# Kernel optimization log

Hardware: AMD Instinct MI355X
Metric: run time of the kernel (lower is better)

## Reference

```python
import jax, jax.numpy as jnp
import numpy as np

B, N, C_IN = 4, 4096, 64
DIM = 64
NKP = 15
K = 32               # neighbor_limits
CONV_RADIUS = 0.1 * 2.0   # conv_radius * rigid_scale (is_deform=False)
KERNEL_RADIUS = 0.12
RECEP = 1.2          # kernel_point_receptive_radius
TRANS_DIM = 128
INF = 1000000.0


def _square_distance(src, dst):
    # src [B,N,3], dst [B,M,3] -> [B,N,M]
    d = -2.0 * jnp.einsum('bnc,bmc->bnm', src, dst)
    d = d + jnp.sum(src * src, -1)[:, :, None]
    d = d + jnp.sum(dst * dst, -1)[:, None, :]
    return d


def _query_ball(xyz, radius):
    # xyz [B,N,3] -> neighbor idx [B,N,K]; out-of-radius mapped to N (shadow)
    n = xyz.shape[1]
    sq = _square_distance(xyz, xyz)
    idx = jnp.broadcast_to(jnp.arange(n, dtype=jnp.int32), sq.shape)
    idx = jnp.where(sq > radius * radius, n, idx)
    idx = jnp.sort(idx, axis=-1)[:, :, :K]
    return idx


def _index_points(points_bcn, idx, pad_val):
    # points [B,C,N], idx [B,N,K] -> [B,N,K,C]; index N hits shadow row = pad_val
    p = jnp.transpose(points_bcn, (0, 2, 1))          # [B,N,C]
    shadow = jnp.full((p.shape[0], 1, p.shape[2]), pad_val, p.dtype)
    p = jnp.concatenate([p, shadow], axis=1)          # [B,N+1,C]
    b_idx = jnp.arange(p.shape[0])[:, None, None]
    return p[b_idx, idx]                              # [B,N,K,C]


def setup_inputs() -> dict:
    key = jax.random.key(0)
    ks = jax.random.split(key, 12)
    pos = jax.random.uniform(ks[0], (B, 3, N), dtype=jnp.float32)
    feat = jax.random.normal(ks[1], (B, C_IN, N), dtype=jnp.float32)
    # kernel points: center point at origin, rest inside kernel_radius ball ('center' mode)
    kp_rest = jax.random.uniform(ks[2], (3, NKP - 1), minval=-KERNEL_RADIUS,
                                 maxval=KERNEL_RADIUS, dtype=jnp.float32)
    kp_pos = jnp.concatenate([jnp.zeros((3, 1), jnp.float32), kp_rest], axis=1)  # [3,NKP]
    s = 0.05
    cb_w = jax.random.normal(ks[3], (DIM, C_IN), jnp.float32) * s
    cb_b = jax.random.normal(ks[4], (DIM,), jnp.float32) * s
    kp_weight = jax.random.normal(ks[5], (NKP, DIM, DIM), jnp.float32) * s
    kp_bias = jax.random.normal(ks[6], (DIM,), jnp.float32) * s
    ce_w = jax.random.normal(ks[7], (C_IN, DIM), jnp.float32) * s
    ce_b = jax.random.normal(ks[8], (C_IN,), jnp.float32) * s
    f1_w = jax.random.normal(ks[9], (2 * DIM, 2 * DIM), jnp.float32) * s
    f1_b = jnp.zeros((2 * DIM,), jnp.float32)
    f2_w = jax.random.normal(ks[10], (TRANS_DIM, 2 * DIM), jnp.float32) * s
    f2_b = jnp.zeros((TRANS_DIM,), jnp.float32)
    return dict(pos=pos, feat=feat, kp_pos=kp_pos, cb_w=cb_w, cb_b=cb_b,
                kp_weight=kp_weight, kp_bias=kp_bias, ce_w=ce_w, ce_b=ce_b,
                f1_w=f1_w, f1_b=f1_b, f2_w=f2_w, f2_b=f2_b)


def reference(pos, feat, kp_pos, cb_w, cb_b, kp_weight, kp_bias, ce_w, ce_b,
              f1_w, f1_b, f2_w, f2_b):
    xyz = jnp.transpose(jax.lax.stop_gradient(pos), (0, 2, 1))       # [B,N,3]
    neighbor_idx = _query_ball(xyz, CONV_RADIUS)                     # [B,N,K]
    # NOTE: with is_deform=False the original code does NOT subtract the center
    # position; rel_neighbor_pos is the absolute gathered positions.
    neighbor_pos = jnp.transpose(_index_points(pos, neighbor_idx, INF),
                                 (0, 3, 1, 2))                        # [B,3,N,K]
    feat0 = jnp.einsum('oc,bcn->bon', cb_w, feat) + cb_b[None, :, None]
    neighbor_feat = _index_points(feat0, neighbor_idx, 0.0)           # [B,N,K,DIM]

    kp_pos_deform = kp_pos.reshape(1, 3, 1, NKP) + 0.0                # offset = 0
    diff = neighbor_pos[..., None] - kp_pos_deform[:, :, :, None, :]  # [B,3,N,K,NKP]
    sq_d = jnp.sum(diff * diff, axis=1)                               # [B,N,K,NKP]
    w = jnp.clip(1.0 - jnp.sqrt(sq_d) / RECEP, 0.0)                   # [B,N,K,NKP]
    w = jnp.transpose(w, (0, 1, 3, 2))                                # [B,N,NKP,K]
    weighted = jnp.einsum('bnpk,bnkc->bnpc', w, neighbor_feat)        # [B,N,NKP,DIM]
    out = jnp.einsum('bnpc,pcd->bnd', weighted, kp_weight) + kp_bias  # [B,N,DIM]
    out = jax.nn.relu(jnp.transpose(out, (0, 2, 1)))                  # [B,DIM,N]
    out = jax.nn.relu(jnp.einsum('oc,bcn->bon', ce_w, out)
                      + ce_b[None, :, None] + feat)                   # [B,C_IN,N]

    fuse_in = jnp.concatenate(
        [jnp.transpose(weighted, (0, 3, 1, 2)),                       # [B,DIM,N,NKP]
         jnp.broadcast_to(out[..., None], (B, DIM, N, NKP))], axis=1) # [B,2DIM,N,NKP]
    h = jax.nn.relu(jnp.einsum('oc,bcnk->bonk', f1_w, fuse_in)
                    + f1_b[None, :, None, None])
    fuse = jax.nn.relu(jnp.einsum('oc,bcnk->bonk', f2_w, h)
                       + f2_b[None, :, None, None])                   # [B,TRANS_DIM,N,NKP]
    return out, kp_pos_deform, fuse
```

## Files before the change

kernel.cpp:

```cpp
#include <hip/hip_runtime.h>
#include <hip/hip_bf16.h>
#include <stdint.h>

#define NPTS 4096
#define NB   4
#define KNN  32
#define NKPT 15

#define OFF_IDX      0ULL
#define OFF_FEAT0    2097152ULL
#define OFF_WEIGHTED 6292480ULL
#define OFF_HO       37749760ULL
#define OFF_W1P      41944064ULL
#define OFF_W2P      41976832ULL
#define OFF_KPWP     42009600ULL

#define OUT_OFF_OUT  0
#define OUT_OFF_KP   1048576
#define OUT_OFF_FUSE 1048621

#define SBU(u) ((u) ^ (((u) >> 3) & 7))

typedef __attribute__((ext_vector_type(8))) short short8v;
typedef __attribute__((ext_vector_type(4))) float f32x4;

__device__ __forceinline__ unsigned short bf16b(float f) {
  __hip_bfloat16 h = __float2bfloat16(f);
  return *(unsigned short*)&h;
}
__device__ __forceinline__ unsigned pkbf(float lo, float hi) {
  return (unsigned)bf16b(lo) | ((unsigned)bf16b(hi) << 16);
}
__device__ __forceinline__ float bflo(unsigned u) { return __uint_as_float(u << 16); }
__device__ __forceinline__ float bfhi(unsigned u) { return __uint_as_float(u & 0xffff0000u); }

__global__ __launch_bounds__(256) void k012(const float* __restrict__ pos,
                                            const float* __restrict__ feat,
                                            const float* __restrict__ cb_w,
                                            const float* __restrict__ cb_b,
                                            const float* __restrict__ f1_w,
                                            const float* __restrict__ f2_w,
                                            const float* __restrict__ kpw,
                                            const float* __restrict__ kp_pos,
                                            int* __restrict__ idx_ws,
                                            float* __restrict__ feat0,
                                            unsigned short* __restrict__ w1p,
                                            unsigned short* __restrict__ w2p,
                                            unsigned short* __restrict__ kpwp,
                                            float* __restrict__ out_kp) {
  __shared__ float cbt[64 * 65];
  const int blk = blockIdx.x;
  if (blk < 4096) {
    const int w = threadIdx.x >> 6, lane = threadIdx.x & 63;
    const int pt = blk * 4 + w;
    const int b = pt >> 12, n = pt & 4095;
    const float* px = pos + (size_t)b * 3 * NPTS;
    const float x0 = px[n], y0 = px[NPTS + n], z0 = px[2 * NPTS + n];
    const float ssrcf = x0 * x0 + y0 * y0 + z0 * z0;
    const double x0d = (double)x0, y0d = (double)y0, z0d = (double)z0;
    const double ssrcd = x0d * x0d + y0d * y0d + z0d * z0d;
    const double RAD = 0.1 * 2.0;
    const double R2 = RAD * RAD;
    const float R2f = (float)R2;
    int cnt = 0;
    int* op = idx_ws + (size_t)pt * KNN;
    for (int ch = 0; ch < 64; ++ch) {
      const int j = ch * 64 + lane;
      const float xj = px[j], yj = px[NPTS + j], zj = px[2 * NPTS + j];
      const float dotf = x0 * xj + y0 * yj + z0 * zj;
      const float sdf  = xj * xj + yj * yj + zj * zj;
      const float sqf  = -2.0f * dotf + ssrcf + sdf;
      const float diff = sqf - R2f;
      bool keep;
      if (__builtin_expect(fabsf(diff) <= 1e-4f, 0)) {
        const double xd = (double)xj, yd = (double)yj, zd = (double)zj;
        const double dd = -2.0 * (x0d * xd + y0d * yd + z0d * zd) + ssrcd
                          + (xd * xd + yd * yd + zd * zd);
        keep = !(dd > R2);
      } else {
        keep = (diff <= 0.0f);
      }
      const unsigned long long m = __ballot(keep);
      if (keep) {
        const int p = cnt + (int)__popcll(m & ((1ULL << lane) - 1ULL));
        if (p < KNN) op[p] = j;
      }
      cnt += (int)__popcll(m);
      if (cnt >= KNN) break;
    }
    const int s = cnt + lane;
    if (s < KNN) op[s] = NPTS;
    return;
  }
  if (blk < 8192) {
    const int t = threadIdx.x;
    #pragma unroll
    for (int q = 0; q < 16; ++q) {
      const int idx = q * 256 + t;
      const int d = idx >> 6, c = idx & 63;
      cbt[c * 65 + d] = cb_w[idx];
    }
    __syncthreads();
    const int ptl = t >> 6, d = t & 63;
    const int pt = (blk - 4096) * 4 + ptl;
    const int b = pt >> 12, n = pt & 4095;
    const float* fp = feat + (size_t)b * 64 * NPTS + n;
    float acc = 0.f;
    #pragma unroll
    for (int c = 0; c < 64; ++c) acc = fmaf(cbt[c * 65 + d], fp[(size_t)c * NPTS], acc);
    acc += cb_b[d];
    feat0[((size_t)b * (NPTS + 1) + n) * 64 + d] = acc;
    return;
  }
  int t = (blk - 8192) * 256 + threadIdx.x;
  if (t < 32768) {
    const int w = t >> 14;
    const int i = t & 16383;
    const int j = i & 7, l = (i >> 3) & 63, kc = (i >> 9) & 3, ot = i >> 11;
    const int o = ot * 16 + (l & 15);
    const int k = kc * 32 + (l >> 4) * 8 + j;
    const float* src = w ? f2_w : f1_w;
    unsigned short* dst = w ? w2p : w1p;
    dst[i] = bf16b(src[o * 128 + k]);
    return;
  }
  t -= 32768;
  if (t < 61440) {
    const int j = t & 7, l = (t >> 3) & 63, nt = (t >> 9) & 3, kc = t >> 11;
    const int k = kc * 32 + (l >> 4) * 8 + j;
    const int d = nt * 16 + (l & 15);
    kpwp[t] = bf16b(kpw[(size_t)k * 64 + d]);
    return;
  }
  t -= 61440;
  if (t < NB * 64) { int b = t >> 6, d = t & 63; feat0[((size_t)b * (NPTS + 1) + NPTS) * 64 + d] = 0.f; return; }
  t -= NB * 64;
  if (t < 45) out_kp[t] = kp_pos[t];
}

__global__ __launch_bounds__(64) void k3_weighted(const float* __restrict__ pos,
                                                  const int* __restrict__ idx_ws,
                                                  const float* __restrict__ feat0,
                                                  const float* __restrict__ kp_pos,
                                                  unsigned short* __restrict__ wbf) {
  __shared__ int   nidx[KNN];
  __shared__ float npx[KNN], npy[KNN], npz[KNN];
  __shared__ float kp[48];
  __shared__ float wl[KNN * 16];
  const int lane = threadIdx.x;
  const int pt = blockIdx.x;
  const int b = pt >> 12;
  if (lane < 45) kp[lane] = kp_pos[lane];
  if (lane < KNN) {
    const int ki = idx_ws[(size_t)pt * KNN + lane];
    nidx[lane] = ki;
    const bool v = ki < NPTS;
    const float* px = pos + (size_t)b * 3 * NPTS;
    npx[lane] = v ? px[ki] : 1000000.0f;
    npy[lane] = v ? px[NPTS + ki] : 1000000.0f;
    npz[lane] = v ? px[2 * NPTS + ki] : 1000000.0f;
  }
  __syncthreads();
  #pragma unroll
  for (int r = 0; r < 8; ++r) {
    const int i = r * 64 + lane;
    const int k = i >> 4, p = i & 15;
    float wv = 0.f;
    if (p < 15) {
      const float dx = npx[k] - kp[p];
      const float dy = npy[k] - kp[15 + p];
      const float dz = npz[k] - kp[30 + p];
      const float d2 = dx * dx + dy * dy + dz * dz;
      wv = fmaxf(1.0f - sqrtf(d2) / 1.2f, 0.f);
    }
    wl[i] = wv;
  }
  __syncthreads();
  float acc[16];
  #pragma unroll
  for (int p = 0; p < 16; ++p) acc[p] = 0.f;
  const float* f0 = feat0 + (size_t)b * (NPTS + 1) * 64 + lane;
  for (int k = 0; k < KNN; ++k) {
    const float f = f0[(size_t)nidx[k] * 64];
    #pragma unroll
    for (int q = 0; q < 4; ++q) {
      const float4 w4 = *(const float4*)&wl[k * 16 + q * 4];
      acc[q * 4 + 0] = fmaf(w4.x, f, acc[q * 4 + 0]);
      acc[q * 4 + 1] = fmaf(w4.y, f, acc[q * 4 + 1]);
      acc[q * 4 + 2] = fmaf(w4.z, f, acc[q * 4 + 2]);
      acc[q * 4 + 3] = fmaf(w4.w, f, acc[q * 4 + 3]);
    }
  }
  unsigned short* wp = wbf + (size_t)pt * NKPT * 64 + lane;
  #pragma unroll
  for (int p = 0; p < 15; ++p) wp[(size_t)p * 64] = bf16b(acc[p]);
}

__global__ __launch_bounds__(256) void k45(const unsigned short* __restrict__ wbf,
                                           const unsigned short* __restrict__ kpwp,
                                           const float* __restrict__ kp_bias,
                                           const float* __restrict__ ce_w,
                                           const float* __restrict__ ce_b,
                                           const float* __restrict__ feat,
                                           const unsigned short* __restrict__ w1p,
                                           const float* __restrict__ f1_b,
                                           float* __restrict__ out,
                                           unsigned short* __restrict__ hOb) {
  __shared__ float r0[64 * 65];
  __shared__ float cwt[64 * 64];
  __shared__ unsigned short outT[64 * 74];
  const int t = threadIdx.x;
  const int b = blockIdx.x >> 6;
  const int n0 = (blockIdx.x & 63) * 64;
  const int wv = t >> 6, lane = t & 63;
  #pragma unroll
  for (int q = 0; q < 16; ++q) {
    const int idx = q * 256 + t;
    cwt[idx] = ce_w[(idx & 63) * 64 + (idx >> 6)];
  }
  const short8v* kf = (const short8v*)kpwp;
  f32x4 acc[4];
  #pragma unroll
  for (int nt = 0; nt < 4; ++nt) acc[nt] = (f32x4){0.f, 0.f, 0.f, 0.f};
  const int m0 = b * 4096 + n0 + wv * 16;
  const unsigned short* ap = wbf + (size_t)(m0 + (lane & 15)) * 960 + (lane >> 4) * 8;
  #pragma unroll 6
  for (int kc = 0; kc < 30; ++kc) {
    const short8v a = *(const short8v*)&ap[kc * 32];
    #pragma unroll
    for (int nt = 0; nt < 4; ++nt)
      acc[nt] = __builtin_amdgcn_mfma_f32_16x16x32_bf16(a, kf[(kc * 4 + nt) * 64 + lane], acc[nt], 0, 0, 0);
  }
  const int rl = wv * 16 + (lane >> 4) * 4;
  #pragma unroll
  for (int nt = 0; nt < 4; ++nt) {
    const int d = nt * 16 + (lane & 15);
    const float bv = kp_bias[d];
    #pragma unroll
    for (int r = 0; r < 4; ++r)
      r0[(rl + r) * 65 + d] = fmaxf(acc[nt][r] + bv, 0.f);
  }
  __syncthreads();
  const int nl = t & 63, og = t >> 6;
  float facc[16];
  #pragma unroll
  for (int j = 0; j < 16; ++j) facc[j] = 0.f;
  for (int c = 0; c < 64; ++c) {
    const float x = r0[nl * 65 + c];
    #pragma unroll
    for (int q = 0; q < 4; ++q) {
      const float4 w4 = *(const float4*)&cwt[c * 64 + og * 16 + q * 4];
      facc[q * 4 + 0] = fmaf(w4.x, x, facc[q * 4 + 0]);
      facc[q * 4 + 1] = fmaf(w4.y, x, facc[q * 4 + 1]);
      facc[q * 4 + 2] = fmaf(w4.z, x, facc[q * 4 + 2]);
      facc[q * 4 + 3] = fmaf(w4.w, x, facc[q * 4 + 3]);
    }
  }
  #pragma unroll
  for (int q = 0; q < 4; ++q) {
    const float4 cb4 = *(const float4*)&ce_b[og * 16 + q * 4];
    const float cbv[4] = {cb4.x, cb4.y, cb4.z, cb4.w};
    #pragma unroll
    for (int j = 0; j < 4; ++j) {
      const int o = og * 16 + q * 4 + j;
      const float fv = feat[((size_t)b * 64 + o) * 4096 + n0 + nl];
      const float v = fmaxf((facc[q * 4 + j] + cbv[j]) + fv, 0.f);
      out[((size_t)b * 64 + o) * 4096 + n0 + nl] = v;
      outT[o * 74 + nl] = bf16b(v);
    }
  }
  __syncthreads();
  const short8v* w1f = (const short8v*)w1p;
  f32x4 hacc[8];
  #pragma unroll
  for (int ot = 0; ot < 8; ++ot) hacc[ot] = (f32x4){0.f, 0.f, 0.f, 0.f};
  const int nw = lane & 15;
  #pragma unroll
  for (int kc2 = 0; kc2 < 2; ++kc2) {
    short8v bfr;
    #pragma unroll
    for (int j = 0; j < 8; ++j)
      bfr[j] = (short)outT[(kc2 * 32 + (lane >> 4) * 8 + j) * 74 + wv * 16 + nw];
    #pragma unroll
    for (int ot = 0; ot < 8; ++ot)
      hacc[ot] = __builtin_amdgcn_mfma_f32_16x16x32_bf16(w1f[(ot * 4 + 2 + kc2) * 64 + lane], bfr, hacc[ot], 0, 0, 0);
  }
  const int rb = (lane >> 4) * 4;
  unsigned short* hp = hOb + ((size_t)b * 4096 + n0 + wv * 16 + nw) * 128;
  #pragma unroll
  for (int ot = 0; ot < 8; ++ot) {
    const int o0 = ot * 16 + rb;
    const float4 b1 = *(const float4*)&f1_b[o0];
    uint2 pk;
    pk.x = pkbf(hacc[ot][0] + b1.x, hacc[ot][1] + b1.y);
    pk.y = pkbf(hacc[ot][2] + b1.z, hacc[ot][3] + b1.w);
    *(uint2*)&hp[o0] = pk;
  }
}

__global__ __launch_bounds__(256, 2) void k6_fuse(const unsigned short* __restrict__ wbf,
                                                  const unsigned short* __restrict__ hOb,
                                                  const unsigned short* __restrict__ w1p,
                                                  const unsigned short* __restrict__ w2p,
                                                  const float* __restrict__ f2_b,
                                                  float* __restrict__ fuse) {
  __shared__ __attribute__((aligned(16))) unsigned short SB[16384];
  __shared__ __attribute__((aligned(8))) unsigned short hOS[12 * 128];
  const int t = threadIdx.x;
  const int blk = blockIdx.x;
  const int b = blk / 480;
  const int ml0 = (blk - b * 480) * 128;
  const size_t M0 = (size_t)blk * 128;
  const int wv = t >> 6, lane = t & 63;
  const short8v* w1f = (const short8v*)w1p;
  const short8v* w2f = (const short8v*)w2p;

  short8v w1r[16];
  #pragma unroll
  for (int ot = 0; ot < 8; ++ot)
    #pragma unroll
    for (int kc = 0; kc < 2; ++kc)
      w1r[ot * 2 + kc] = w1f[(ot * 4 + kc) * 64 + lane];

  #pragma unroll
  for (int q = 0; q < 4; ++q) {
    const int chunk = q * 256 + t;
    const int m = chunk >> 3, a = chunk & 7;
    const uint4 pk = *(const uint4*)&wbf[(M0 + m) * 64 + a * 8];
    const int kc = a >> 2, hi = a & 3;
    const int u = ((m >> 4) * 4 + kc) * 64 + hi * 16 + (m & 15);
    *(uint4*)&SB[SBU(u) * 8] = pk;
  }
  const int nmin = ml0 / 15;
  #pragma unroll
  for (int q = 0; q < 3; ++q) {
    const int idx = q * 256 + t;
    const int row = idx >> 6, pr = idx & 63;
    int n = nmin + row;
    if (n > 4095) n = 4095;
    ((unsigned*)hOS)[idx] = ((const unsigned*)(hOb + ((size_t)b * 4096 + n) * 128))[pr];
  }
  __syncthreads();

  short8v xf[4];
  #pragma unroll
  for (int mt = 0; mt < 2; ++mt)
    #pragma unroll
    for (int kc = 0; kc < 2; ++kc) {
      const int u = ((wv * 2 + mt) * 4 + kc) * 64 + lane;
      xf[mt * 2 + kc] = *(const short8v*)&SB[SBU(u) * 8];
    }

  const int rb = (lane >> 4) * 4;
  const int dnA = (ml0 + wv * 32 + (lane & 15)) / 15 - nmin;
  const int dnB = (ml0 + wv * 32 + 16 + (lane & 15)) / 15 - nmin;
  f32x4 acc[8][2];
  #pragma unroll
  for (int ot = 0; ot < 8; ++ot) {
    const uint2 pa = *(const uint2*)&hOS[dnA * 128 + ot * 16 + rb];
    const uint2 pb = *(const uint2*)&hOS[dnB * 128 + ot * 16 + rb];
    acc[ot][0] = (f32x4){bflo(pa.x), bfhi(pa.x), bflo(pa.y), bfhi(pa.y)};
    acc[ot][1] = (f32x4){bflo(pb.x), bfhi(pb.x), bflo(pb.y), bfhi(pb.y)};
  }
  short8v w2a[16];
  #pragma unroll
  for (int i = 0; i < 16; ++i) w2a[i] = w2f[i * 64 + lane];

  #pragma unroll
  for (int kc = 0; kc < 2; ++kc) {
    #pragma unroll
    for (int ot = 0; ot < 8; ++ot) {
      acc[ot][0] = __builtin_amdgcn_mfma_f32_16x16x32_bf16(w1r[ot * 2 + kc], xf[kc],     acc[ot][0], 0, 0, 0);
      acc[ot][1] = __builtin_amdgcn_mfma_f32_16x16x32_bf16(w1r[ot * 2 + kc], xf[2 + kc], acc[ot][1], 0, 0, 0);
    }
  }
  #pragma unroll
  for (int ot = 0; ot < 8; ++ot) {
    const int o0 = ot * 16 + rb;
    const int kc = o0 >> 5, hi = (o0 >> 3) & 3, j0 = o0 & 7;
    #pragma unroll
    for (int mt = 0; mt < 2; ++mt) {
      const f32x4 h = acc[ot][mt];
      const float h0 = fmaxf(h[0], 0.f);
      const float h1 = fmaxf(h[1], 0.f);
      const float h2 = fmaxf(h[2], 0.f);
      const float h3 = fmaxf(h[3], 0.f);
      const int u = ((wv * 2 + mt) * 4 + kc) * 64 + hi * 16 + (lane & 15);
      uint2 pk;
      pk.x = pkbf(h0, h1);
      pk.y = pkbf(h2, h3);
      *(uint2*)&SB[SBU(u) * 8 + j0] = pk;
    }
  }
  short8v w2b[16];
  #pragma unroll
  for (int i = 0; i < 16; ++i) w2b[i] = w2f[(16 + i) * 64 + lane];

  short8v hf[8];
  #pragma unroll
  for (int mt = 0; mt < 2; ++mt)
    #pragma unroll
    for (int kc = 0; kc < 4; ++kc) {
      const int u = ((wv * 2 + mt) * 4 + kc) * 64 + lane;
      hf[mt * 4 + kc] = *(const short8v*)&SB[SBU(u) * 8];
    }
  #pragma unroll
  for (int ot = 0; ot < 8; ++ot) {
    acc[ot][0] = (f32x4){0.f, 0.f, 0.f, 0.f};
    acc[ot][1] = (f32x4){0.f, 0.f, 0.f, 0.f};
  }
  #pragma unroll
  for (int kc = 0; kc < 4; ++kc) {
    #pragma unroll
    for (int ot = 0; ot < 4; ++ot) {
      acc[ot][0] = __builtin_amdgcn_mfma_f32_16x16x32_bf16(w2a[ot * 4 + kc], hf[kc],     acc[ot][0], 0, 0, 0);
      acc[ot][1] = __builtin_amdgcn_mfma_f32_16x16x32_bf16(w2a[ot * 4 + kc], hf[4 + kc], acc[ot][1], 0, 0, 0);
    }
  }
  #pragma unroll
  for (int kc = 0; kc < 4; ++kc) {
    #pragma unroll
    for (int ot = 4; ot < 8; ++ot) {
      acc[ot][0] = __builtin_amdgcn_mfma_f32_16x16x32_bf16(w2b[(ot - 4) * 4 + kc], hf[kc],     acc[ot][0], 0, 0, 0);
      acc[ot][1] = __builtin_amdgcn_mfma_f32_16x16x32_bf16(w2b[(ot - 4) * 4 + kc], hf[4 + kc], acc[ot][1], 0, 0, 0);
    }
  }
  float* fp0 = fuse + (size_t)b * 128 * 61440 + ml0 + wv * 32 + (lane & 15);
  #pragma unroll
  for (int ot = 0; ot < 8; ++ot) {
    const int o0 = ot * 16 + rb;
    const float4 b2 = *(const float4*)&f2_b[o0];
    const float bv[4] = {b2.x, b2.y, b2.z, b2.w};
    #pragma unroll
    for (int mt = 0; mt < 2; ++mt) {
      const f32x4 vacc = acc[ot][mt];
      #pragma unroll
      for (int r = 0; r < 4; ++r)
        fp0[(size_t)(o0 + r) * 61440 + mt * 16] = fmaxf(vacc[r] + bv[r], 0.f);
    }
  }
}

extern "C" void kernel_launch(void* const* d_in, const int* in_sizes, int n_in,
                              void* d_out, int out_size, void* d_ws, size_t ws_size,
                              hipStream_t stream) {
  const float* pos     = (const float*)d_in[0];
  const float* feat    = (const float*)d_in[1];
  const float* kp_pos  = (const float*)d_in[2];
  const float* cb_w    = (const float*)d_in[3];
  const float* cb_b    = (const float*)d_in[4];
  const float* kpw     = (const float*)d_in[5];
  const float* kp_bias = (const float*)d_in[6];
  const float* ce_w    = (const float*)d_in[7];
  const float* ce_b    = (const float*)d_in[8];
  const float* f1_w    = (const float*)d_in[9];
  const float* f1_b    = (const float*)d_in[10];
  const float* f2_w    = (const float*)d_in[11];
  const float* f2_b    = (const float*)d_in[12];
  float* out = (float*)d_out;
  char* ws = (char*)d_ws;
  int*   idx_ws   = (int*)(ws + OFF_IDX);
  float* feat0    = (float*)(ws + OFF_FEAT0);
  unsigned short* wbf  = (unsigned short*)(ws + OFF_WEIGHTED);
  unsigned short* hOb  = (unsigned short*)(ws + OFF_HO);
  unsigned short* w1p  = (unsigned short*)(ws + OFF_W1P);
  unsigned short* w2p  = (unsigned short*)(ws + OFF_W2P);
  unsigned short* kpwp = (unsigned short*)(ws + OFF_KPWP);

  k012<<<8562, 256, 0, stream>>>(pos, feat, cb_w, cb_b, f1_w, f2_w, kpw, kp_pos,
                                 idx_ws, feat0, w1p, w2p, kpwp, out + OUT_OFF_KP);
  k3_weighted<<<16384, 64, 0, stream>>>(pos, idx_ws, feat0, kp_pos, wbf);
  k45<<<256, 256, 0, stream>>>(wbf, kpwp, kp_bias, ce_w, ce_b, feat, w1p, f1_b,
                               out + OUT_OFF_OUT, hOb);
  k6_fuse<<<1920, 256, 0, stream>>>(wbf, hOb, w1p, w2p, f2_b, out + OUT_OFF_FUSE);
}
```

Measured before the change: 140.1 us.

## Split fuse MLP work across waves by output channels instead of point columns

Each wave in k6_fuse now owns a 32-channel slice of the outputs and loops over all 128 point columns of the block, where before it owned 32 columns and all 128 channels. Each wave therefore holds only its slice of the W1 and W2 weight fragments in registers, which lowers register pressure. The hidden activations are written to a separate shared buffer, and a block-wide barrier now sits between the two layers. Output stores also change shape: each lane now writes 16-column row segments across its channel slice.

```diff
diff --git a/kernel.cpp b/kernel.cpp
--- a/kernel.cpp
+++ b/kernel.cpp
@@ -305,6 +305,7 @@
                                                   const float* __restrict__ f2_b,
                                                   float* __restrict__ fuse) {
   __shared__ __attribute__((aligned(16))) unsigned short SB[16384];
+  __shared__ __attribute__((aligned(16))) unsigned short HB[16384];
   __shared__ __attribute__((aligned(8))) unsigned short hOS[12 * 128];
   const int t = threadIdx.x;
   const int blk = blockIdx.x;
@@ -312,15 +313,22 @@
   const int ml0 = (blk - b * 480) * 128;
   const size_t M0 = (size_t)blk * 128;
   const int wv = t >> 6, lane = t & 63;
+  const int cl = lane & 15, rb = (lane >> 4) * 4;
   const short8v* w1f = (const short8v*)w1p;
   const short8v* w2f = (const short8v*)w2p;
 
-  short8v w1r[16];
-  #pragma unroll
-  for (int ot = 0; ot < 8; ++ot)
+  short8v w1a[4];
+  #pragma unroll
+  for (int oi = 0; oi < 2; ++oi)
     #pragma unroll
     for (int kc = 0; kc < 2; ++kc)
-      w1r[ot * 2 + kc] = w1f[(ot * 4 + kc) * 64 + lane];
+      w1a[oi * 2 + kc] = w1f[((wv * 2 + oi) * 4 + kc) * 64 + lane];
+  short8v w2r[8];
+  #pragma unroll
+  for (int oi = 0; oi < 2; ++oi)
+    #pragma unroll
+    for (int kc = 0; kc < 4; ++kc)
+      w2r[oi * 4 + kc] = w2f[((wv * 2 + oi) * 4 + kc) * 64 + lane];
 
   #pragma unroll
   for (int q = 0; q < 4; ++q) {
@@ -342,101 +350,57 @@
   }
   __syncthreads();
 
-  short8v xf[4];
-  #pragma unroll
-  for (int mt = 0; mt < 2; ++mt)
-    #pragma unroll
-    for (int kc = 0; kc < 2; ++kc) {
-      const int u = ((wv * 2 + mt) * 4 + kc) * 64 + lane;
-      xf[mt * 2 + kc] = *(const short8v*)&SB[SBU(u) * 8];
-    }
-
-  const int rb = (lane >> 4) * 4;
-  const int dnA = (ml0 + wv * 32 + (lane & 15)) / 15 - nmin;
-  const int dnB = (ml0 + wv * 32 + 16 + (lane & 15)) / 15 - nmin;
-  f32x4 acc[8][2];
-  #pragma unroll
-  for (int ot = 0; ot < 8; ++ot) {
-    const uint2 pa = *(const uint2*)&hOS[dnA * 128 + ot * 16 + rb];
-    const uint2 pb = *(const uint2*)&hOS[dnB * 128 + ot * 16 + rb];
-    acc[ot][0] = (f32x4){bflo(pa.x), bfhi(pa.x), bflo(pa.y), bfhi(pa.y)};
-    acc[ot][1] = (f32x4){bflo(pb.x), bfhi(pb.x), bflo(pb.y), bfhi(pb.y)};
-  }
-  short8v w2a[16];
-  #pragma unroll
-  for (int i = 0; i < 16; ++i) w2a[i] = w2f[i * 64 + lane];
-
-  #pragma unroll
-  for (int kc = 0; kc < 2; ++kc) {
-    #pragma unroll
-    for (int ot = 0; ot < 8; ++ot) {
-      acc[ot][0] = __builtin_amdgcn_mfma_f32_16x16x32_bf16(w1r[ot * 2 + kc], xf[kc],     acc[ot][0], 0, 0, 0);
-      acc[ot][1] = __builtin_amdgcn_mfma_f32_16x16x32_bf16(w1r[ot * 2 + kc], xf[2 + kc], acc[ot][1], 0, 0, 0);
-    }
-  }
-  #pragma unroll
-  for (int ot = 0; ot < 8; ++ot) {
-    const int o0 = ot * 16 + rb;
-    const int kc = o0 >> 5, hi = (o0 >> 3) & 3, j0 = o0 & 7;
-    #pragma unroll
-    for (int mt = 0; mt < 2; ++mt) {
-      const f32x4 h = acc[ot][mt];
-      const float h0 = fmaxf(h[0], 0.f);
-      const float h1 = fmaxf(h[1], 0.f);
-      const float h2 = fmaxf(h[2], 0.f);
-      const float h3 = fmaxf(h[3], 0.f);
-      const int u = ((wv * 2 + mt) * 4 + kc) * 64 + hi * 16 + (lane & 15);
+  #pragma unroll
+  for (int mt = 0; mt < 8; ++mt) {
+    const int dn = (ml0 + mt * 16 + cl) / 15 - nmin;
+    const uint2 p0 = *(const uint2*)&hOS[dn * 128 + wv * 32 + rb];
+    const uint2 p1 = *(const uint2*)&hOS[dn * 128 + wv * 32 + 16 + rb];
+    f32x4 a0 = (f32x4){bflo(p0.x), bfhi(p0.x), bflo(p0.y), bfhi(p0.y)};
+    f32x4 a1 = (f32x4){bflo(p1.x), bfhi(p1.x), bflo(p1.y), bfhi(p1.y)};
+    const short8v x0 = *(const short8v*)&SB[SBU((mt * 4 + 0) * 64 + lane) * 8];
+    const short8v x1 = *(const short8v*)&SB[SBU((mt * 4 + 1) * 64 + lane) * 8];
+    a0 = __builtin_amdgcn_mfma_f32_16x16x32_bf16(w1a[0], x0, a0, 0, 0, 0);
+    a0 = __builtin_amdgcn_mfma_f32_16x16x32_bf16(w1a[1], x1, a0, 0, 0, 0);
+    a1 = __builtin_amdgcn_mfma_f32_16x16x32_bf16(w1a[2], x0, a1, 0, 0, 0);
+    a1 = __builtin_amdgcn_mfma_f32_16x16x32_bf16(w1a[3], x1, a1, 0, 0, 0);
+    #pragma unroll
+    for (int oi = 0; oi < 2; ++oi) {
+      const f32x4 h = oi ? a1 : a0;
+      const int c0 = wv * 32 + oi * 16 + rb;
+      const int kc = c0 >> 5, hi = (c0 >> 3) & 3, j0 = c0 & 7;
       uint2 pk;
-      pk.x = pkbf(h0, h1);
-      pk.y = pkbf(h2, h3);
-      *(uint2*)&SB[SBU(u) * 8 + j0] = pk;
-    }
-  }
-  short8v w2b[16];
-  #pragma unroll
-  for (int i = 0; i < 16; ++i) w2b[i] = w2f[(16 + i) * 64 + lane];
-
-  short8v hf[8];
-  #pragma unroll
-  for (int mt = 0; mt < 2; ++mt)
-    #pragma unroll
-    for (int kc = 0; kc < 4; ++kc) {
-      const int u = ((wv * 2 + mt) * 4 + kc) * 64 + lane;
-      hf[mt * 4 + kc] = *(const short8v*)&SB[SBU(u) * 8];
-    }
-  #pragma unroll
-  for (int ot = 0; ot < 8; ++ot) {
-    acc[ot][0] = (f32x4){0.f, 0.f, 0.f, 0.f};
-    acc[ot][1] = (f32x4){0.f, 0.f, 0.f, 0.f};
-  }
-  #pragma unroll
-  for (int kc = 0; kc < 4; ++kc) {
-    #pragma unroll
-    for (int ot = 0; ot < 4; ++ot) {
-      acc[ot][0] = __builtin_amdgcn_mfma_f32_16x16x32_bf16(w2a[ot * 4 + kc], hf[kc],     acc[ot][0], 0, 0, 0);
-      acc[ot][1] = __builtin_amdgcn_mfma_f32_16x16x32_bf16(w2a[ot * 4 + kc], hf[4 + kc], acc[ot][1], 0, 0, 0);
-    }
-  }
-  #pragma unroll
-  for (int kc = 0; kc < 4; ++kc) {
-    #pragma unroll
-    for (int ot = 4; ot < 8; ++ot) {
-      acc[ot][0] = __builtin_amdgcn_mfma_f32_16x16x32_bf16(w2b[(ot - 4) * 4 + kc], hf[kc],     acc[ot][0], 0, 0, 0);
-      acc[ot][1] = __builtin_amdgcn_mfma_f32_16x16x32_bf16(w2b[(ot - 4) * 4 + kc], hf[4 + kc], acc[ot][1], 0, 0, 0);
-    }
-  }
-  float* fp0 = fuse + (size_t)b * 128 * 61440 + ml0 + wv * 32 + (lane & 15);
-  #pragma unroll
-  for (int ot = 0; ot < 8; ++ot) {
-    const int o0 = ot * 16 + rb;
-    const float4 b2 = *(const float4*)&f2_b[o0];
-    const float bv[4] = {b2.x, b2.y, b2.z, b2.w};
-    #pragma unroll
-    for (int mt = 0; mt < 2; ++mt) {
-      const f32x4 vacc = acc[ot][mt];
-      #pragma unroll
-      for (int r = 0; r < 4; ++r)
-        fp0[(size_t)(o0 + r) * 61440 + mt * 16] = fmaxf(vacc[r] + bv[r], 0.f);
+      pk.x = pkbf(fmaxf(h[0], 0.f), fmaxf(h[1], 0.f));
+      pk.y = pkbf(fmaxf(h[2], 0.f), fmaxf(h[3], 0.f));
+      const int u = (mt * 4 + kc) * 64 + hi * 16 + cl;
+      *(uint2*)&HB[SBU(u) * 8 + j0] = pk;
+    }
+  }
+  __syncthreads();
+
+  const float4 b2a = *(const float4*)&f2_b[wv * 32 + rb];
+  const float4 b2b = *(const float4*)&f2_b[wv * 32 + 16 + rb];
+  float* fblk = fuse + (size_t)b * 128 * 61440 + ml0;
+  #pragma unroll
+  for (int mt = 0; mt < 8; ++mt) {
+    short8v h0 = *(const short8v*)&HB[SBU((mt * 4 + 0) * 64 + lane) * 8];
+    short8v h1 = *(const short8v*)&HB[SBU((mt * 4 + 1) * 64 + lane) * 8];
+    short8v h2 = *(const short8v*)&HB[SBU((mt * 4 + 2) * 64 + lane) * 8];
+    short8v h3 = *(const short8v*)&HB[SBU((mt * 4 + 3) * 64 + lane) * 8];
+    f32x4 a0 = (f32x4){0.f, 0.f, 0.f, 0.f};
+    f32x4 a1 = (f32x4){0.f, 0.f, 0.f, 0.f};
+    a0 = __builtin_amdgcn_mfma_f32_16x16x32_bf16(w2r[0], h0, a0, 0, 0, 0);
+    a0 = __builtin_amdgcn_mfma_f32_16x16x32_bf16(w2r[1], h1, a0, 0, 0, 0);
+    a0 = __builtin_amdgcn_mfma_f32_16x16x32_bf16(w2r[2], h2, a0, 0, 0, 0);
+    a0 = __builtin_amdgcn_mfma_f32_16x16x32_bf16(w2r[3], h3, a0, 0, 0, 0);
+    a1 = __builtin_amdgcn_mfma_f32_16x16x32_bf16(w2r[4], h0, a1, 0, 0, 0);
+    a1 = __builtin_amdgcn_mfma_f32_16x16x32_bf16(w2r[5], h1, a1, 0, 0, 0);
+    a1 = __builtin_amdgcn_mfma_f32_16x16x32_bf16(w2r[6], h2, a1, 0, 0, 0);
+    a1 = __builtin_amdgcn_mfma_f32_16x16x32_bf16(w2r[7], h3, a1, 0, 0, 0);
+    const int colc = mt * 16 + cl;
+    #pragma unroll
+    for (int r = 0; r < 4; ++r) {
+      fblk[(size_t)(wv * 32 + rb + r) * 61440 + colc]      = fmaxf(a0[r] + ((const float*)&b2a)[r], 0.f);
+      fblk[(size_t)(wv * 32 + 16 + rb + r) * 61440 + colc] = fmaxf(a1[r] + ((const float*)&b2b)[r], 0.f);
     }
   }
 }
```

Measured after the change: 137.3 us. 1.02x faster.
